# Performance work log

Measured on AMD Instinct MI355X. Metric: run time of the kernel, lower is better.

## Reference

```python
import jax, jax.numpy as jnp
import numpy as np

N_NODES = 50000

def _gcn_conv(x, W, b, src, dst, num_nodes):
    # PyG GCNConv: linear transform, then D^{-1/2} A_hat D^{-1/2} aggregation (A_hat has self-loops).
    xw = x @ W                                   # [N, out]
    ones = jnp.ones(src.shape[0], dtype=x.dtype)
    deg = jax.ops.segment_sum(ones, dst, num_segments=num_nodes)  # in-degree incl. self loop
    dinv = jnp.where(deg > 0, jax.lax.rsqrt(deg), 0.0)
    norm = dinv[src] * dinv[dst]                 # [E]
    msg = xw[src] * norm[:, None]                # [E, out] gather + scale
    out = jax.ops.segment_sum(msg, dst, num_segments=num_nodes)   # scatter-add
    return out + b

def _add_self_loops(edge_index, num_nodes):
    loop = jnp.arange(num_nodes, dtype=edge_index.dtype)
    src = jnp.concatenate([edge_index[0], loop])
    dst = jnp.concatenate([edge_index[1], loop])
    return src, dst

def setup_inputs() -> dict:
    key = jax.random.key(0)
    k = jax.random.split(key, 6)
    in_dim, hid_dim, out_dim = 256, 128, 64
    n_edges = 800000
    x = jax.random.normal(k[0], (N_NODES, in_dim), dtype=jnp.float32)
    edge_index = jax.random.randint(k[1], (2, n_edges), 0, N_NODES, dtype=jnp.int64)
    W1 = jax.random.normal(k[2], (in_dim, hid_dim), dtype=jnp.float32) / np.sqrt(in_dim)
    b1 = jnp.zeros((hid_dim,), dtype=jnp.float32)
    W2 = jax.random.normal(k[3], (hid_dim, out_dim), dtype=jnp.float32) / np.sqrt(hid_dim)
    b2 = jnp.zeros((out_dim,), dtype=jnp.float32)
    return {"x": x, "edge_index": edge_index, "W1": W1, "b1": b1, "W2": W2, "b2": b2}

def reference(x, edge_index, W1, b1, W2, b2):
    src, dst = _add_self_loops(edge_index, N_NODES)
    h = jnp.tanh(_gcn_conv(x, W1, b1, src, dst, N_NODES))
    out = _gcn_conv(h, W2, b2, src, dst, N_NODES)
    return out
```

## Files before the change

kernel.cpp:

```cpp
#include <hip/hip_runtime.h>

#define INDIM 256
#define HID 128
#define OUTD 64

typedef _Float16 f16x8 __attribute__((ext_vector_type(8)));
typedef float    f32x4 __attribute__((ext_vector_type(4)));

__global__ __launch_bounds__(256) void k_setup(const float* __restrict__ W1, const float* __restrict__ W2,
                                               _Float16* __restrict__ W1t, _Float16* __restrict__ W2t,
                                               int* __restrict__ counts, int* __restrict__ cursor, int M) {
    constexpr int NW1 = HID * INDIM;
    constexpr int NW2 = OUTD * HID;
    int id = blockIdx.x * 256 + threadIdx.x;
    if (id < NW1) {
        int n = id / INDIM, k = id % INDIM;
        W1t[id] = (_Float16)W1[k * HID + n];
    } else if (id < NW1 + NW2) {
        int j = id - NW1;
        int n = j / HID, k = j % HID;
        W2t[j] = (_Float16)W2[k * OUTD + n];
    } else {
        int i = id - NW1 - NW2;
        if (i < M) { counts[i] = 0; cursor[i] = 0; }
    }
}


__global__ __launch_bounds__(256) void k_count(const int* __restrict__ dst, int* __restrict__ counts, int E) {
    int e = blockIdx.x * 256 + threadIdx.x;
    if (e < E) atomicAdd(&counts[dst[e]], 1);
}

__global__ __launch_bounds__(256) void k_breduce(const int* __restrict__ counts, int* __restrict__ bsum, int M) {
    __shared__ int s[256];
    int tid = threadIdx.x;
    int i = blockIdx.x * 256 + tid;
    s[tid] = (i < M) ? counts[i] : 0;
    __syncthreads();
#pragma unroll
    for (int off = 128; off > 0; off >>= 1) {
        if (tid < off) s[tid] += s[tid + off];
        __syncthreads();
    }
    if (tid == 0) bsum[blockIdx.x] = s[0];
}

__global__ __launch_bounds__(256) void k_bscan(int* __restrict__ bsum, int NB) {
    __shared__ int s[256];
    int tid = threadIdx.x;
    int v = (tid < NB) ? bsum[tid] : 0;
    s[tid] = v;
    __syncthreads();
#pragma unroll
    for (int off = 1; off < 256; off <<= 1) {
        int t = (tid >= off) ? s[tid - off] : 0;
        __syncthreads();
        s[tid] += t;
        __syncthreads();
    }
    if (tid < NB) bsum[tid] = s[tid] - v;
}

__global__ __launch_bounds__(256) void k_scan_final(const int* __restrict__ counts, const int* __restrict__ bsum,
                                                    int* __restrict__ row_start, float* __restrict__ dinv, int M) {
    __shared__ int s[256];
    int tid = threadIdx.x;
    int i = blockIdx.x * 256 + tid;
    int v = (i < M) ? counts[i] : 0;
    s[tid] = v;
    __syncthreads();
#pragma unroll
    for (int off = 1; off < 256; off <<= 1) {
        int t = (tid >= off) ? s[tid - off] : 0;
        __syncthreads();
        s[tid] += t;
        __syncthreads();
    }
    if (i < M) {
        int excl = bsum[blockIdx.x] + s[tid] - v;
        row_start[i] = excl;
        dinv[i] = rsqrtf(1.0f + (float)v);
        if (i == M - 1) row_start[M] = excl + v;
    }
}

__global__ __launch_bounds__(256) void k_fill(const int* __restrict__ src, const int* __restrict__ dst,
                                              const int* __restrict__ row_start, int* __restrict__ cursor,
                                              int* __restrict__ edge_src, int E) {
    int e = blockIdx.x * 256 + threadIdx.x;
    if (e >= E) return;
    int d = dst[e];
    int pos = row_start[d] + atomicAdd(&cursor[d], 1);
    edge_src[pos] = src[e];
}

template <int BN, int K, typename AT>
__global__ __launch_bounds__(256) void k_gemm_mfma(
    const AT* __restrict__ X, const _Float16* __restrict__ Wt,
    const float* __restrict__ dinv, _Float16* __restrict__ XW16, int M)
{
    constexpr int BM = 64;
    constexpr int BK = 32;
    constexpr int NT = BN / 16;
    constexpr int LDK = BK + 8;

    __shared__ __align__(16) _Float16 As[BM][LDK];
    __shared__ __align__(16) _Float16 Bs[BN][LDK];

    const int tid  = threadIdx.x;
    const int wave = tid >> 6;
    const int lane = tid & 63;
    const int m    = lane & 15;
    const int q    = lane >> 4;
    const int rb   = blockIdx.x * BM;

    f32x4 acc[NT];
#pragma unroll
    for (int t = 0; t < NT; t++) acc[t] = (f32x4){0.f, 0.f, 0.f, 0.f};

    for (int kt = 0; kt < K; kt += BK) {
        if (kt) __syncthreads();
        if constexpr (sizeof(AT) == 4) {
#pragma unroll
            for (int i = 0; i < BM * 8 / 256; i++) {
                int ch  = tid + i * 256;
                int row = ch >> 3;
                int c4  = ch & 7;
                int gr  = rb + row;
                float4 v = make_float4(0.f, 0.f, 0.f, 0.f);
                if (gr < M) v = *(const float4*)((const float*)X + (long)gr * K + kt + c4 * 4);
                _Float16* p = &As[row][c4 * 4];
                p[0] = (_Float16)v.x; p[1] = (_Float16)v.y;
                p[2] = (_Float16)v.z; p[3] = (_Float16)v.w;
            }
        } else {
            int row = tid >> 2;
            int c8  = tid & 3;
            int gr  = rb + row;
            uint4 v = make_uint4(0u, 0u, 0u, 0u);
            if (gr < M) v = *(const uint4*)((const _Float16*)X + (long)gr * K + kt + c8 * 8);
            *(uint4*)(&As[row][c8 * 8]) = v;
        }
#pragma unroll
        for (int i = 0; i < BN * 8 / 256; i++) {
            int ch = tid + i * 256;
            int n  = ch >> 3;
            int c4 = ch & 7;
            *(ushort4*)(&Bs[n][c4 * 4]) =
                *(const ushort4*)(Wt + (long)n * K + kt + c4 * 4);
        }
        __syncthreads();

        f16x8 af = *(const f16x8*)(&As[wave * 16 + m][q * 8]);
#pragma unroll
        for (int t = 0; t < NT; t++) {
            f16x8 bf = *(const f16x8*)(&Bs[t * 16 + m][q * 8]);
            acc[t] = __builtin_amdgcn_mfma_f32_16x16x32_f16(af, bf, acc[t], 0, 0, 0);
        }
    }

    int row0 = rb + wave * 16 + q * 4;
#pragma unroll
    for (int r = 0; r < 4; r++) {
        int row = row0 + r;
        if (row < M) {
            float di = dinv[row];
#pragma unroll
            for (int t = 0; t < NT; t++) {
                XW16[(long)row * BN + t * 16 + m] = (_Float16)(acc[t][r] * di);
            }
        }
    }
}

template <int F, bool TANH, typename OutT>
__global__ __launch_bounds__(256) void k_agg_csr(const int* __restrict__ row_start,
                                                 const int* __restrict__ edge_src,
                                                 const _Float16* __restrict__ feat,
                                                 const float* __restrict__ bias,
                                                 const float* __restrict__ dinv,
                                                 OutT* __restrict__ out, int M) {
    constexpr int LPN = F / 8;
    constexpr int NPB = 256 / LPN;
    int n = blockIdx.x * NPB + threadIdx.x / LPN;
    int c = threadIdx.x % LPN;
    if (n >= M) return;
    int beg = row_start[n], end = row_start[n + 1];

    f16x8 self = *(const f16x8*)(feat + (long)n * F + c * 8);
    float acc[8];
#pragma unroll
    for (int k = 0; k < 8; k++) acc[k] = (float)self[k];

    int j = beg;
    for (; j + 1 < end; j += 2) {
        int s0 = edge_src[j], s1 = edge_src[j + 1];
        f16x8 v0 = *(const f16x8*)(feat + (long)s0 * F + c * 8);
        f16x8 v1 = *(const f16x8*)(feat + (long)s1 * F + c * 8);
#pragma unroll
        for (int k = 0; k < 8; k++) acc[k] += (float)v0[k] + (float)v1[k];
    }
    if (j < end) {
        int s = edge_src[j];
        f16x8 v = *(const f16x8*)(feat + (long)s * F + c * 8);
#pragma unroll
        for (int k = 0; k < 8; k++) acc[k] += (float)v[k];
    }

    float di = dinv[n];
#pragma unroll
    for (int k = 0; k < 8; k++) acc[k] = bias[c * 8 + k] + di * acc[k];
    if (TANH) {
#pragma unroll
        for (int k = 0; k < 8; k++) acc[k] = tanhf(acc[k]);
    }
    if constexpr (sizeof(OutT) == 2) {
        f16x8 o;
#pragma unroll
        for (int k = 0; k < 8; k++) o[k] = (_Float16)acc[k];
        *(f16x8*)((_Float16*)out + (long)n * F + c * 8) = o;
    } else {
        float* p = (float*)out + (long)n * F + c * 8;
        *(float4*)(p)     = make_float4(acc[0], acc[1], acc[2], acc[3]);
        *(float4*)(p + 4) = make_float4(acc[4], acc[5], acc[6], acc[7]);
    }
}

extern "C" void kernel_launch(void* const* d_in, const int* in_sizes, int n_in,
                              void* d_out, int out_size, void* d_ws, size_t ws_size,
                              hipStream_t stream) {
    const float* x  = (const float*)d_in[0];
    const int*   ei = (const int*)d_in[1];
    const float* W1 = (const float*)d_in[2];
    const float* b1 = (const float*)d_in[3];
    const float* W2 = (const float*)d_in[4];
    const float* b2 = (const float*)d_in[5];
    float* out = (float*)d_out;

    const int M = in_sizes[0] / INDIM;
    const int E = in_sizes[1] / 2;
    const int* srcp = ei;
    const int* dstp = ei + E;

    const int Mp = (M + 63) & ~63;
    const int NB = (M + 255) / 256;

    float*     dinv      = (float*)d_ws;
    int*       counts    = (int*)(dinv + Mp);
    int*       cursor    = counts + Mp;
    int*       row_start = cursor + Mp;
    int*       bsum      = row_start + Mp;
    _Float16*  W1t       = (_Float16*)(bsum + 256);
    _Float16*  W2t       = W1t + HID * INDIM;
    int*       edge_src  = (int*)(W2t + OUTD * HID);
    _Float16*  xw16      = (_Float16*)(edge_src + E);
    _Float16*  h16       = xw16 + (long)M * HID;
    _Float16*  hw16      = xw16;

    {
        int total = HID * INDIM + OUTD * HID + M;
        k_setup<<<(total + 255) / 256, 256, 0, stream>>>(W1, W2, W1t, W2t, counts, cursor, M);
    }

    k_count<<<(E + 255) / 256, 256, 0, stream>>>(dstp, counts, E);
    k_breduce<<<NB, 256, 0, stream>>>(counts, bsum, M);
    k_bscan<<<1, 256, 0, stream>>>(bsum, NB);
    k_scan_final<<<NB, 256, 0, stream>>>(counts, bsum, row_start, dinv, M);
    k_fill<<<(E + 255) / 256, 256, 0, stream>>>(srcp, dstp, row_start, cursor, edge_src, E);

    k_gemm_mfma<HID, INDIM, float><<<(M + 63) / 64, 256, 0, stream>>>(x, W1t, dinv, xw16, M);
    k_agg_csr<HID, true, _Float16><<<(M + 15) / 16, 256, 0, stream>>>(row_start, edge_src, xw16, b1, dinv, h16, M);

    k_gemm_mfma<OUTD, HID, _Float16><<<(M + 63) / 64, 256, 0, stream>>>(h16, W2t, dinv, hw16, M);
    k_agg_csr<OUTD, false, float><<<(M + 31) / 32, 256, 0, stream>>>(row_start, edge_src, hw16, b2, dinv, out, M);
}
```

Baseline: 254.6 us.

## Build CSR via two-level binned counting sort with shared-memory atomics

Replaces the per-node global-atomic count, three-kernel scan, and global-atomic fill with a bucketed counting sort. Edges are first histogrammed into 256-node bins using shared-memory atomics and scattered into a binned buffer. A per-bin kernel then does local counting and placement in shared memory to produce row_start, dinv and edge_src. This aims to remove contended global atomics and cut the number of launches. In exchange it adds an extra int2 intermediate buffer written and read once, and it supports at most 256 bins, which caps M at 65536.

New measurement: 230.8 us. -9.4%, faster.

```diff
diff --git a/kernel.cpp b/kernel.cpp
--- a/kernel.cpp
+++ b/kernel.cpp
@@ -3,13 +3,15 @@
 #define INDIM 256
 #define HID 128
 #define OUTD 64
+#define BINSHIFT 8
+#define MAXBIN 256
 
 typedef _Float16 f16x8 __attribute__((ext_vector_type(8)));
 typedef float    f32x4 __attribute__((ext_vector_type(4)));
 
 __global__ __launch_bounds__(256) void k_setup(const float* __restrict__ W1, const float* __restrict__ W2,
                                                _Float16* __restrict__ W1t, _Float16* __restrict__ W2t,
-                                               int* __restrict__ counts, int* __restrict__ cursor, int M) {
+                                               int* __restrict__ bin_counts) {
     constexpr int NW1 = HID * INDIM;
     constexpr int NW2 = OUTD * HID;
     int id = blockIdx.x * 256 + threadIdx.x;
@@ -22,34 +24,32 @@
         W2t[j] = (_Float16)W2[k * OUTD + n];
     } else {
         int i = id - NW1 - NW2;
-        if (i < M) { counts[i] = 0; cursor[i] = 0; }
-    }
-}
-
-
-__global__ __launch_bounds__(256) void k_count(const int* __restrict__ dst, int* __restrict__ counts, int E) {
-    int e = blockIdx.x * 256 + threadIdx.x;
-    if (e < E) atomicAdd(&counts[dst[e]], 1);
-}
-
-__global__ __launch_bounds__(256) void k_breduce(const int* __restrict__ counts, int* __restrict__ bsum, int M) {
+        if (i < MAXBIN) bin_counts[i] = 0;
+    }
+}
+
+__global__ __launch_bounds__(256) void k_hist(const int* __restrict__ dst, int* __restrict__ bin_counts, int E) {
+    __shared__ int h[MAXBIN];
+    int tid = threadIdx.x;
+    h[tid] = 0;
+    __syncthreads();
+    int base = blockIdx.x * 2048;
+#pragma unroll
+    for (int i = 0; i < 8; i++) {
+        int e = base + i * 256 + tid;
+        if (e < E) atomicAdd(&h[dst[e] >> BINSHIFT], 1);
+    }
+    __syncthreads();
+    int v = h[tid];
+    if (v) atomicAdd(&bin_counts[tid], v);
+}
+
+__global__ __launch_bounds__(256) void k_bscan(const int* __restrict__ bin_counts,
+                                               int* __restrict__ bin_start, int* __restrict__ bin_cursor,
+                                               int* __restrict__ row_start, int NBIN, int M, int E) {
     __shared__ int s[256];
     int tid = threadIdx.x;
-    int i = blockIdx.x * 256 + tid;
-    s[tid] = (i < M) ? counts[i] : 0;
-    __syncthreads();
-#pragma unroll
-    for (int off = 128; off > 0; off >>= 1) {
-        if (tid < off) s[tid] += s[tid + off];
-        __syncthreads();
-    }
-    if (tid == 0) bsum[blockIdx.x] = s[0];
-}
-
-__global__ __launch_bounds__(256) void k_bscan(int* __restrict__ bsum, int NB) {
-    __shared__ int s[256];
-    int tid = threadIdx.x;
-    int v = (tid < NB) ? bsum[tid] : 0;
+    int v = (tid < NBIN) ? bin_counts[tid] : 0;
     s[tid] = v;
     __syncthreads();
 #pragma unroll
@@ -59,16 +59,65 @@
         s[tid] += t;
         __syncthreads();
     }
-    if (tid < NB) bsum[tid] = s[tid] - v;
-}
-
-__global__ __launch_bounds__(256) void k_scan_final(const int* __restrict__ counts, const int* __restrict__ bsum,
-                                                    int* __restrict__ row_start, float* __restrict__ dinv, int M) {
+    if (tid < NBIN) {
+        int excl = s[tid] - v;
+        bin_start[tid] = excl;
+        bin_cursor[tid] = excl;
+    }
+    if (tid == 0) {
+        bin_start[NBIN] = E;
+        row_start[M] = E;
+    }
+}
+
+__global__ __launch_bounds__(256) void k_binfill(const int* __restrict__ src, const int* __restrict__ dst,
+                                                 int* __restrict__ bin_cursor, int2* __restrict__ binned, int E) {
+    __shared__ int h[MAXBIN];
+    __shared__ int rb[MAXBIN];
+    int tid = threadIdx.x;
+    h[tid] = 0;
+    __syncthreads();
+    int base = blockIdx.x * 2048;
+    int es[8], ed[8], rk[8];
+#pragma unroll
+    for (int i = 0; i < 8; i++) {
+        int e = base + i * 256 + tid;
+        if (e < E) {
+            es[i] = src[e];
+            ed[i] = dst[e];
+            rk[i] = atomicAdd(&h[ed[i] >> BINSHIFT], 1);
+        } else {
+            ed[i] = -1;
+        }
+    }
+    __syncthreads();
+    int c = h[tid];
+    if (c) rb[tid] = atomicAdd(&bin_cursor[tid], c);
+    __syncthreads();
+#pragma unroll
+    for (int i = 0; i < 8; i++) {
+        if (ed[i] >= 0) {
+            binned[rb[ed[i] >> BINSHIFT] + rk[i]] = make_int2(es[i], ed[i]);
+        }
+    }
+}
+
+__global__ __launch_bounds__(256) void k_csr(const int2* __restrict__ binned, const int* __restrict__ bin_start,
+                                             int* __restrict__ row_start, float* __restrict__ dinv,
+                                             int* __restrict__ edge_src, int M) {
+    __shared__ int cnt[256];
     __shared__ int s[256];
-    int tid = threadIdx.x;
-    int i = blockIdx.x * 256 + tid;
-    int v = (i < M) ? counts[i] : 0;
-    s[tid] = v;
+    __shared__ int cur[256];
+    int b = blockIdx.x, tid = threadIdx.x;
+    int beg = bin_start[b], end = bin_start[b + 1];
+    cnt[tid] = 0;
+    __syncthreads();
+    for (int i = beg + tid; i < end; i += 256) {
+        atomicAdd(&cnt[binned[i].y & 255], 1);
+    }
+    __syncthreads();
+    int c = cnt[tid];
+    s[tid] = c;
     __syncthreads();
 #pragma unroll
     for (int off = 1; off < 256; off <<= 1) {
@@ -77,22 +126,19 @@
         s[tid] += t;
         __syncthreads();
     }
-    if (i < M) {
-        int excl = bsum[blockIdx.x] + s[tid] - v;
-        row_start[i] = excl;
-        dinv[i] = rsqrtf(1.0f + (float)v);
-        if (i == M - 1) row_start[M] = excl + v;
-    }
-}
-
-__global__ __launch_bounds__(256) void k_fill(const int* __restrict__ src, const int* __restrict__ dst,
-                                              const int* __restrict__ row_start, int* __restrict__ cursor,
-                                              int* __restrict__ edge_src, int E) {
-    int e = blockIdx.x * 256 + threadIdx.x;
-    if (e >= E) return;
-    int d = dst[e];
-    int pos = row_start[d] + atomicAdd(&cursor[d], 1);
-    edge_src[pos] = src[e];
+    int start = beg + s[tid] - c;
+    int node = (b << BINSHIFT) + tid;
+    if (node < M) {
+        row_start[node] = start;
+        dinv[node] = rsqrtf(1.0f + (float)c);
+    }
+    cur[tid] = start;
+    __syncthreads();
+    for (int i = beg + tid; i < end; i += 256) {
+        int2 e = binned[i];
+        int pos = atomicAdd(&cur[e.y & 255], 1);
+        edge_src[pos] = e.x;
+    }
 }
 
 template <int BN, int K, typename AT>
@@ -243,31 +289,32 @@
     const int* srcp = ei;
     const int* dstp = ei + E;
 
-    const int Mp = (M + 63) & ~63;
-    const int NB = (M + 255) / 256;
-
-    float*     dinv      = (float*)d_ws;
-    int*       counts    = (int*)(dinv + Mp);
-    int*       cursor    = counts + Mp;
-    int*       row_start = cursor + Mp;
-    int*       bsum      = row_start + Mp;
-    _Float16*  W1t       = (_Float16*)(bsum + 256);
-    _Float16*  W2t       = W1t + HID * INDIM;
-    int*       edge_src  = (int*)(W2t + OUTD * HID);
-    _Float16*  xw16      = (_Float16*)(edge_src + E);
-    _Float16*  h16       = xw16 + (long)M * HID;
-    _Float16*  hw16      = xw16;
+    const int Mp   = (M + 63) & ~63;
+    const int NBIN = (M + 255) >> BINSHIFT;
+
+    float*     dinv       = (float*)d_ws;
+    int*       row_start  = (int*)(dinv + Mp);
+    int*       bin_start  = row_start + Mp;
+    int*       bin_cursor = bin_start + 258;
+    int*       bin_counts = bin_cursor + MAXBIN;
+    _Float16*  W1t        = (_Float16*)(bin_counts + MAXBIN);
+    _Float16*  W2t        = W1t + HID * INDIM;
+    int2*      binned     = (int2*)(W2t + OUTD * HID);
+    int*       edge_src   = (int*)(binned + E);
+    _Float16*  xw16       = (_Float16*)(edge_src + E);
+    _Float16*  h16        = xw16 + (long)M * HID;
+    _Float16*  hw16       = xw16;
+
+    const int NWE = (E + 2047) / 2048;
 
     {
-        int total = HID * INDIM + OUTD * HID + M;
-        k_setup<<<(total + 255) / 256, 256, 0, stream>>>(W1, W2, W1t, W2t, counts, cursor, M);
-    }
-
-    k_count<<<(E + 255) / 256, 256, 0, stream>>>(dstp, counts, E);
-    k_breduce<<<NB, 256, 0, stream>>>(counts, bsum, M);
-    k_bscan<<<1, 256, 0, stream>>>(bsum, NB);
-    k_scan_final<<<NB, 256, 0, stream>>>(counts, bsum, row_start, dinv, M);
-    k_fill<<<(E + 255) / 256, 256, 0, stream>>>(srcp, dstp, row_start, cursor, edge_src, E);
+        int total = HID * INDIM + OUTD * HID + MAXBIN;
+        k_setup<<<(total + 255) / 256, 256, 0, stream>>>(W1, W2, W1t, W2t, bin_counts);
+    }
+    k_hist<<<NWE, 256, 0, stream>>>(dstp, bin_counts, E);
+    k_bscan<<<1, 256, 0, stream>>>(bin_counts, bin_start, bin_cursor, row_start, NBIN, M, E);
+    k_binfill<<<NWE, 256, 0, stream>>>(srcp, dstp, bin_cursor, binned, E);
+    k_csr<<<NBIN, 256, 0, stream>>>(binned, bin_start, row_start, dinv, edge_src, M);
 
     k_gemm_mfma<HID, INDIM, float><<<(M + 63) / 64, 256, 0, stream>>>(x, W1t, dinv, xw16, M);
     k_agg_csr<HID, true, _Float16><<<(M + 15) / 16, 256, 0, stream>>>(row_start, edge_src, xw16, b1, dinv, h16, M);
```
